# Performance work log

Hardware: AMD Instinct MI355X
Metric: run time of the kernel (lower is better)

## Reference

```python
import jax, jax.numpy as jnp
import numpy as np

THRESHOLD = 0.05
TOP_N = 512
NMS_THR = 0.6
POST_TOP_N = 100
MIN_SIZE = 0.0
N_CLASS = 8
IMG_SIZE = (256.0, 256.0, 64.0)
B, C, H, W, D = 4, 8, 128, 128, 32


def _pairwise_iou3d(b):
    # b: [K, 6] in xyzxyz; returns [K, K] volumetric IoU
    lo, hi = b[:, :3], b[:, 3:]
    ilo = jnp.maximum(lo[:, None, :], lo[None, :, :])
    ihi = jnp.minimum(hi[:, None, :], hi[None, :, :])
    inter = jnp.prod(jnp.maximum(ihi - ilo, 0.0), axis=-1)
    vol = jnp.prod(jnp.maximum(hi - lo, 0.0), axis=-1)
    return inter / (vol[:, None] + vol[None, :] - inter + 1e-9)


def _nms_keep(boxes, scores, thr):
    # greedy NMS; scores == -1 marks invalid entries. Returns bool keep mask [K].
    K = boxes.shape[0]
    order = jnp.argsort(-scores)
    b = boxes[order]
    s = scores[order]
    iou = _pairwise_iou3d(b)
    idx = jnp.arange(K)

    def body(i, keep):
        sup = (iou[i] > thr) & keep[i] & (idx > i)
        return keep & ~sup

    keep = jax.lax.fori_loop(0, K, body, s > 0.0)
    return jnp.zeros(K, dtype=bool).at[order].set(keep)


def _forward(location, cls_pred, box_pred, center_pred):
    Bb, Cc = cls_pred.shape[0], cls_pred.shape[1]
    N = cls_pred.shape[2] * cls_pred.shape[3] * cls_pred.shape[4]
    # [B, C, H, W, D] -> [B, N, C]
    cls = jax.nn.sigmoid(cls_pred).transpose(0, 2, 3, 4, 1).reshape(Bb, N, Cc)
    ctr = jax.nn.sigmoid(center_pred).transpose(0, 2, 3, 4, 1).reshape(Bb, N)
    box = box_pred.transpose(0, 2, 3, 4, 1).reshape(Bb, N, 6)

    candid = cls > THRESHOLD                      # [B, N, C]
    scores = cls * ctr[:, :, None]                # centerness-weighted
    flat = jnp.where(candid, scores, -1.0).reshape(Bb, N * Cc)
    vals, idx = jax.lax.top_k(flat, TOP_N)        # fixed-size stand-in for mask+topk
    valid = vals > 0.0                            # matches torch clamp(count, top_n)

    loc_idx = idx // Cc                           # flattened spatial location
    class_id = idx % Cc + 1                       # labels are 1-based
    bsel = jnp.take_along_axis(box, loc_idx[..., None], axis=1)   # [B, K, 6]
    lsel = location[loc_idx]                                      # [B, K, 3]
    det = jnp.concatenate([lsel - bsel[..., :3], lsel + bsel[..., 3:]], axis=-1)

    # BoxList.clip to image volume
    full = jnp.concatenate([jnp.asarray(IMG_SIZE), jnp.asarray(IMG_SIZE)]).astype(det.dtype) - 1.0
    det = jnp.clip(det, 0.0, full)

    score = jnp.where(valid, jnp.sqrt(jnp.where(valid, vals, 1.0)), 0.0)

    # remove_small_boxes
    sides = det[..., 3:] - det[..., :3]
    valid = valid & jnp.all(sides >= MIN_SIZE, axis=-1)

    # per-class greedy NMS (decisions are non-differentiable; torch detaches anyway)
    det_ng = jax.lax.stop_gradient(det)
    score_ng = jax.lax.stop_gradient(score)

    def per_image(b_i, s_i, c_i, v_i):
        def per_class(j):
            m = v_i & (c_i == j)
            return _nms_keep(b_i, jnp.where(m, s_i, -1.0), NMS_THR) & m
        return jnp.any(jax.vmap(per_class)(jnp.arange(1, N_CLASS + 1)), axis=0)

    valid = jax.vmap(per_image)(det_ng, score_ng, class_id, valid)

    # post_top_n selection (kthvalue threshold == keep top post_top_n scores)
    fv, fi = jax.lax.top_k(jnp.where(valid, score_ng, -1.0), POST_TOP_N)
    fvalid = fv > 0.0
    fbox = jnp.take_along_axis(det, fi[..., None], axis=1) * fvalid[..., None]
    fscore = jnp.where(fvalid, jnp.take_along_axis(score, fi, axis=1), 0.0)
    flabel = jnp.where(fvalid, jnp.take_along_axis(class_id, fi, axis=1), 0)
    return fbox, fscore, flabel, fvalid


def setup_inputs() -> dict:
    key = jax.random.key(0)
    k1, k2, k3, k4 = jax.random.split(key, 4)
    N = H * W * D
    location = jax.random.uniform(k1, (N, 3), dtype=jnp.float32) * jnp.asarray(IMG_SIZE, jnp.float32)
    cls_pred = jax.random.normal(k2, (B, C, H, W, D), dtype=jnp.float32) - 2.0  # realistic logits
    box_pred = jax.random.uniform(k3, (B, 6, H, W, D), dtype=jnp.float32) * 20.0  # positive extents
    center_pred = jax.random.normal(k4, (B, 1, H, W, D), dtype=jnp.float32)
    return {"location": location, "cls_pred": cls_pred, "box_pred": box_pred, "center_pred": center_pred}


def reference(location, cls_pred, box_pred, center_pred):
    return _forward(location, cls_pred, box_pred, center_pred)
```

## Files before the change

### kernel.cpp

```cpp
#include <hip/hip_runtime.h>

#define NB 4
#define NC 8
#define NLOC 524288
#define TOPN 512
#define POST 100
#define NBIN 8192
#define SELBINS 4096
#define SCAP 4096
#define CAP 16384
#define LCAP 2048
#define NMS_THR 0.6f
#define CAND_THR 0.05f
#define SPEC_THR 0.5f

typedef unsigned long long ull;

#define OFF_CNT    0
#define OFF_OVF    16
#define OFF_KEYS   64
#define ZERO_BYTES 32

__device__ __forceinline__ float sigmoidf_(float x) {
    return 1.0f / (1.0f + expf(-x));
}

__global__ __launch_bounds__(256) void gather_spec(const float* __restrict__ cls,
                                                   const float* __restrict__ ctr,
                                                   ull* __restrict__ keys,
                                                   unsigned int* __restrict__ counts,
                                                   unsigned int* __restrict__ ovf) {
    __shared__ ull lkeys[LCAP];
    __shared__ unsigned int lcnt;
    __shared__ unsigned int lbase;
    const int b = blockIdx.y;
    if (threadIdx.x == 0) lcnt = 0;
    __syncthreads();

    const int n0 = (blockIdx.x * blockDim.x + threadIdx.x) * 4;
    const float4 cv = *(const float4*)(ctr + (size_t)b * NLOC + n0);
    float4 cl[NC];
    #pragma unroll
    for (int c = 0; c < NC; ++c)
        cl[c] = *(const float4*)(cls + ((size_t)b * NC + c) * NLOC + n0);

    #pragma unroll
    for (int j = 0; j < 4; ++j) {
        bool any = false;
        #pragma unroll
        for (int c = 0; c < NC; ++c) any |= (((const float*)&cl[c])[j] > 0.0f);
        if (any) {
            const float sc = sigmoidf_(((const float*)&cv)[j]);
            #pragma unroll
            for (int c = 0; c < NC; ++c) {
                const float x = ((const float*)&cl[c])[j];
                if (x > 0.0f) {
                    const float p = sigmoidf_(x) * sc;
                    if (p > SPEC_THR) {
                        const unsigned pos = atomicAdd(&lcnt, 1u);
                        if (pos < LCAP) {
                            const unsigned flat = (unsigned)((n0 + j) * NC + c);
                            lkeys[pos] = ((ull)__float_as_uint(p) << 32) | (unsigned)(~flat);
                        }
                    }
                }
            }
        }
    }
    __syncthreads();
    const unsigned m = lcnt;
    if (threadIdx.x == 0) {
        const unsigned stored = (m > LCAP) ? LCAP : m;
        lbase = atomicAdd(&counts[b], stored);
        if (m > LCAP) ovf[b] = 1;
    }
    __syncthreads();
    const unsigned stored = (m > LCAP) ? LCAP : m;
    const unsigned base = lbase;
    for (unsigned i = threadIdx.x; i < stored; i += blockDim.x) {
        const unsigned pos = base + i;
        if (pos < CAP) keys[(size_t)b * CAP + pos] = lkeys[i];
    }
}

__global__ __launch_bounds__(1024) void select_nms_kernel(const float* __restrict__ cls,
                                                          const float* __restrict__ ctr,
                                                          ull* __restrict__ keys,
                                                          unsigned int* __restrict__ counts,
                                                          const unsigned int* __restrict__ ovf,
                                                          const float* __restrict__ loc,
                                                          const float* __restrict__ box,
                                                          float* __restrict__ out) {
    __shared__ union SU {
        struct { unsigned int hist[SELBINS]; ull surv[SCAP]; } sel;
        unsigned int fhist[NBIN];
        struct { float sd[TOPN * 6]; float ss[TOPN]; int scl[TOPN];
                 int keep[TOPN]; int clist[NC][TOPN]; int wcnt[NC]; } nms;
    } u;
    __shared__ ull tk[TOPN];
    __shared__ unsigned int scnt;
    __shared__ int cut_s;

    const int b = blockIdx.x, t = threadIdx.x;

    {
        const unsigned cnt0 = counts[b];
        const bool bad = !(cnt0 >= TOPN && cnt0 <= CAP && ovf[b] == 0);
        if (bad) {
            for (int i = t; i < NBIN; i += 1024) u.fhist[i] = 0;
            __syncthreads();
            for (int n = t; n < NLOC; n += 1024) {
                const float sc = sigmoidf_(ctr[(size_t)b * NLOC + n]);
                #pragma unroll
                for (int c = 0; c < NC; ++c) {
                    const float s = sigmoidf_(cls[((size_t)b * NC + c) * NLOC + n]);
                    if (s > CAND_THR) atomicAdd(&u.fhist[__float_as_uint(s * sc) >> 17], 1u);
                }
            }
            __syncthreads();
            if (t == 0) {
                unsigned cum = 0; int bin = 0;
                for (int i = NBIN - 1; i >= 0; --i) {
                    cum += u.fhist[i];
                    if (cum >= TOPN) { bin = i; break; }
                }
                cut_s = bin;
                counts[b] = 0;
            }
            __syncthreads();
            const unsigned cb2 = (unsigned)cut_s;
            for (int n = t; n < NLOC; n += 1024) {
                const float sc = sigmoidf_(ctr[(size_t)b * NLOC + n]);
                #pragma unroll
                for (int c = 0; c < NC; ++c) {
                    const float s = sigmoidf_(cls[((size_t)b * NC + c) * NLOC + n]);
                    if (s > CAND_THR) {
                        const unsigned bits = __float_as_uint(s * sc);
                        if ((bits >> 17) >= cb2) {
                            const unsigned pos = atomicAdd(&counts[b], 1u);
                            if (pos < CAP)
                                keys[(size_t)b * CAP + pos] =
                                    ((ull)bits << 32) | (unsigned)(~(unsigned)(n * NC + c));
                        }
                    }
                }
            }
        }
    }
    __syncthreads();

    const int M = (int)min(counts[b], (unsigned)CAP);

    for (int i = t; i < SELBINS; i += 1024) u.sel.hist[i] = 0;
    if (t == 0) scnt = 0;
    if (t < TOPN) tk[t] = 0;
    __syncthreads();
    for (int i = t; i < M; i += 1024) {
        const unsigned hi = (unsigned)(keys[(size_t)b * CAP + i] >> 32);
        const int off = (int)hi - 0x3F000000;
        int bin = (off < 0) ? 0 : (off >> 11);
        if (bin > SELBINS - 1) bin = SELBINS - 1;
        atomicAdd(&u.sel.hist[bin], 1u);
    }
    __syncthreads();

    if (t < 64) {
        unsigned s = 0;
        for (int i = 0; i < 64; ++i)
            s += u.sel.hist[t * 64 + ((i + t) & 63)];
        unsigned suf = s;
        #pragma unroll
        for (int d = 1; d < 64; d <<= 1) {
            const unsigned o = __shfl_down(suf, d);
            suf += (t + d < 64) ? o : 0u;
        }
        const ull mask = __ballot(suf >= TOPN);
        unsigned nxt = __shfl_down(suf, 1);
        if (t == 63) nxt = 0;
        if (mask == 0ull) {
            if (t == 0) cut_s = 0;
        } else {
            const int L = 63 - __builtin_clzll(mask);
            if (t == L) {
                unsigned cum = nxt;
                int c = L * 64;
                for (int i = 63; i >= 0; --i) {
                    cum += u.sel.hist[L * 64 + i];
                    if (cum >= TOPN) { c = L * 64 + i; break; }
                }
                cut_s = c;
            }
        }
    }
    __syncthreads();

    const int cb = cut_s;
    for (int i = t; i < M; i += 1024) {
        const ull k = keys[(size_t)b * CAP + i];
        const unsigned hi = (unsigned)(k >> 32);
        const int off = (int)hi - 0x3F000000;
        int bin = (off < 0) ? 0 : (off >> 11);
        if (bin > SELBINS - 1) bin = SELBINS - 1;
        if (bin >= cb) {
            const unsigned p = atomicAdd(&scnt, 1u);
            if (p < SCAP) u.sel.surv[p] = k;
        }
    }
    __syncthreads();

    const unsigned sc_final = scnt;
    if (sc_final <= (unsigned)SCAP) {
        const int S = (int)sc_final;
        for (int i = t; i < S; i += 1024) {
            const ull ke = u.sel.surv[i];
            int r = 0;
            for (int j = 0; j < S; ++j) r += (u.sel.surv[j] > ke) ? 1 : 0;
            if (r < TOPN) tk[r] = ke;
        }
    } else {
        for (int i = t; i < M; i += 1024) {
            const ull ke = keys[(size_t)b * CAP + i];
            int r = 0;
            for (int j = 0; j < M; ++j) r += (keys[(size_t)b * CAP + j] > ke) ? 1 : 0;
            if (r < TOPN) tk[r] = ke;
        }
    }
    __syncthreads();

    volatile int* keep = u.nms.keep;
    if (t < TOPN) {
        const ull k = tk[t];
        const unsigned bits = (unsigned)(k >> 32);
        const float val = __uint_as_float(bits);
        int valid = (val > 0.0f) ? 1 : 0;
        const unsigned flat = ~(unsigned)(k & 0xffffffffu);
        int n = 0, c = 0;
        if (valid) { n = (int)(flat >> 3); c = (int)(flat & 7u); }
        const float lx = loc[n * 3 + 0], ly = loc[n * 3 + 1], lz = loc[n * 3 + 2];
        const float* bp = box + (size_t)b * 6 * NLOC + n;
        const float b0 = bp[0];
        const float b1 = bp[(size_t)NLOC];
        const float b2 = bp[2 * (size_t)NLOC];
        const float b3 = bp[3 * (size_t)NLOC];
        const float b4 = bp[4 * (size_t)NLOC];
        const float b5 = bp[5 * (size_t)NLOC];
        const float d0 = fminf(fmaxf(lx - b0, 0.0f), 255.0f);
        const float d1 = fminf(fmaxf(ly - b1, 0.0f), 255.0f);
        const float d2 = fminf(fmaxf(lz - b2, 0.0f), 63.0f);
        const float d3 = fminf(fmaxf(lx + b3, 0.0f), 255.0f);
        const float d4 = fminf(fmaxf(ly + b4, 0.0f), 255.0f);
        const float d5 = fminf(fmaxf(lz + b5, 0.0f), 63.0f);
        if (d3 - d0 < 0.0f || d4 - d1 < 0.0f || d5 - d2 < 0.0f) valid = 0;
        u.nms.sd[t * 6 + 0] = d0; u.nms.sd[t * 6 + 1] = d1; u.nms.sd[t * 6 + 2] = d2;
        u.nms.sd[t * 6 + 3] = d3; u.nms.sd[t * 6 + 4] = d4; u.nms.sd[t * 6 + 5] = d5;
        u.nms.ss[t] = (val > 0.0f) ? sqrtf(val) : 0.0f;
        u.nms.scl[t] = c + 1;
        keep[t] = valid;
    }
    __syncthreads();

    if (t < TOPN) {
        const int w = t >> 6, lane = t & 63;
        const int myclass = w + 1;
        const float* sd = u.nms.sd;
        int cnt = 0;
        for (int j0 = 0; j0 < TOPN; j0 += 64) {
            const int j = j0 + lane;
            const bool pred = (u.nms.scl[j] == myclass) && (keep[j] != 0);
            const ull m = __ballot(pred);
            if (pred) {
                const int pos = cnt + __popcll(m & ((1ull << lane) - 1ull));
                u.nms.clist[w][pos] = j;
            }
            cnt += __popcll(m);
        }
        __threadfence_block();

        for (int i = 0; i < cnt; ++i) {
            const int gi = u.nms.clist[w][i];
            if (!keep[gi]) continue;
            const float lx0 = sd[gi * 6 + 0], ly0 = sd[gi * 6 + 1], lz0 = sd[gi * 6 + 2];
            const float hx0 = sd[gi * 6 + 3], hy0 = sd[gi * 6 + 4], hz0 = sd[gi * 6 + 5];
            const float vol0 = fmaxf(hx0 - lx0, 0.0f) * fmaxf(hy0 - ly0, 0.0f) * fmaxf(hz0 - lz0, 0.0f);
            for (int e = i + 1 + lane; e < cnt; e += 64) {
                const int gj = u.nms.clist[w][e];
                if (keep[gj]) {
                    const float lx1 = sd[gj * 6 + 0], ly1 = sd[gj * 6 + 1], lz1 = sd[gj * 6 + 2];
                    const float hx1 = sd[gj * 6 + 3], hy1 = sd[gj * 6 + 4], hz1 = sd[gj * 6 + 5];
                    const float ix = fminf(hx0, hx1) - fmaxf(lx0, lx1);
                    const float iy = fminf(hy0, hy1) - fmaxf(ly0, ly1);
                    const float iz = fminf(hz0, hz1) - fmaxf(lz0, lz1);
                    const float inter = fmaxf(ix, 0.0f) * fmaxf(iy, 0.0f) * fmaxf(iz, 0.0f);
                    const float vol1 = fmaxf(hx1 - lx1, 0.0f) * fmaxf(hy1 - ly1, 0.0f) * fmaxf(hz1 - lz1, 0.0f);
                    const float iou = inter / (vol0 + vol1 - inter + 1e-9f);
                    if (iou > NMS_THR) keep[gj] = 0;
                }
            }
            __threadfence_block();
        }
    }
    __syncthreads();

    if (t < TOPN) {
        const int w = t >> 6, lane = t & 63;
        const ull km = __ballot(keep[t] != 0);
        if (lane == 0) u.nms.wcnt[w] = __popcll(km);
        __threadfence_block();
        (void)km;
    }
    __syncthreads();
    if (t < TOPN) {
        const int w = t >> 6, lane = t & 63;
        const ull km = __ballot(keep[t] != 0);
        int before = 0, total = 0;
        #pragma unroll
        for (int w2 = 0; w2 < NC; ++w2) {
            total += u.nms.wcnt[w2];
            if (w2 < w) before += u.nms.wcnt[w2];
        }
        const int myrank = before + __popcll(km & ((1ull << lane) - 1ull));

        float* fbox = out;
        float* fscore = out + NB * POST * 6;
        float* flabel = out + NB * POST * 7;
        float* fvalid = out + NB * POST * 8;

        if (keep[t] && myrank < POST) {
            #pragma unroll
            for (int k = 0; k < 6; ++k) fbox[(b * POST + myrank) * 6 + k] = u.nms.sd[t * 6 + k];
            fscore[b * POST + myrank] = u.nms.ss[t];
            flabel[b * POST + myrank] = (float)u.nms.scl[t];
            fvalid[b * POST + myrank] = 1.0f;
        }
        const int tc = (total < POST) ? total : POST;
        if (t >= tc && t < POST) {
            #pragma unroll
            for (int k = 0; k < 6; ++k) fbox[(b * POST + t) * 6 + k] = 0.0f;
            fscore[b * POST + t] = 0.0f;
            flabel[b * POST + t] = 0.0f;
            fvalid[b * POST + t] = 0.0f;
        }
    }
}

extern "C" void kernel_launch(void* const* d_in, const int* in_sizes, int n_in,
                              void* d_out, int out_size, void* d_ws, size_t ws_size,
                              hipStream_t stream) {
    const float* location = (const float*)d_in[0];
    const float* cls_pred = (const float*)d_in[1];
    const float* box_pred = (const float*)d_in[2];
    const float* ctr_pred = (const float*)d_in[3];

    char* ws = (char*)d_ws;
    unsigned int* counts = (unsigned int*)(ws + OFF_CNT);
    unsigned int* ovf    = (unsigned int*)(ws + OFF_OVF);
    ull*          keys   = (ull*)(ws + OFF_KEYS);

    hipMemsetAsync(d_ws, 0, ZERO_BYTES, stream);

    gather_spec<<<dim3(NLOC / 1024, NB), 256, 0, stream>>>(cls_pred, ctr_pred, keys, counts, ovf);
    select_nms_kernel<<<NB, 1024, 0, stream>>>(cls_pred, ctr_pred, keys, counts, ovf,
                                               location, box_pred, (float*)d_out);
}
```

Before: 100.7 us.

## Register-cache keys, wave-local register NMS, 8-wide gather, fast exp

The gather kernel now has each thread process 8 locations instead of 4, halving the grid, and sigmoid uses the fast __expf intrinsic. The select kernel loads all CAP keys into registers once with 128-bit loads, so the histogram and survivor passes no longer read global memory twice. Per-class NMS keeps each box in registers and broadcasts the pivot box by shuffle with a ballot-tracked keep mask when a class has at most 128 candidates, replacing the shared-memory volatile loop. Risks: the fast exp can change scores near thresholds, and holding 16 keys per thread raises register pressure in a 1024-thread block.

```diff
diff --git a/kernel.cpp b/kernel.cpp
--- a/kernel.cpp
+++ b/kernel.cpp
@@ -9,6 +9,7 @@
 #define SELBINS 4096
 #define SCAP 4096
 #define CAP 16384
+#define KPT 16
 #define LCAP 2048
 #define NMS_THR 0.6f
 #define CAND_THR 0.05f
@@ -22,7 +23,7 @@
 #define ZERO_BYTES 32
 
 __device__ __forceinline__ float sigmoidf_(float x) {
-    return 1.0f / (1.0f + expf(-x));
+    return 1.0f / (1.0f + __expf(-x));
 }
 
 __global__ __launch_bounds__(256) void gather_spec(const float* __restrict__ cls,
@@ -37,30 +38,41 @@
     if (threadIdx.x == 0) lcnt = 0;
     __syncthreads();
 
-    const int n0 = (blockIdx.x * blockDim.x + threadIdx.x) * 4;
-    const float4 cv = *(const float4*)(ctr + (size_t)b * NLOC + n0);
-    float4 cl[NC];
+    const int n0 = (blockIdx.x * blockDim.x + threadIdx.x) * 8;
+    const float4* cvp = (const float4*)(ctr + (size_t)b * NLOC + n0);
+    const float4 cv0 = cvp[0], cv1 = cvp[1];
+    float4 cl0[NC], cl1[NC];
     #pragma unroll
-    for (int c = 0; c < NC; ++c)
-        cl[c] = *(const float4*)(cls + ((size_t)b * NC + c) * NLOC + n0);
+    for (int c = 0; c < NC; ++c) {
+        const float4* p = (const float4*)(cls + ((size_t)b * NC + c) * NLOC + n0);
+        cl0[c] = p[0];
+        cl1[c] = p[1];
+    }
 
     #pragma unroll
-    for (int j = 0; j < 4; ++j) {
-        bool any = false;
-        #pragma unroll
-        for (int c = 0; c < NC; ++c) any |= (((const float*)&cl[c])[j] > 0.0f);
-        if (any) {
-            const float sc = sigmoidf_(((const float*)&cv)[j]);
+    for (int h = 0; h < 2; ++h) {
+        const float4 cv = h ? cv1 : cv0;
+        #pragma unroll
+        for (int j = 0; j < 4; ++j) {
+            bool any = false;
             #pragma unroll
             for (int c = 0; c < NC; ++c) {
-                const float x = ((const float*)&cl[c])[j];
-                if (x > 0.0f) {
-                    const float p = sigmoidf_(x) * sc;
-                    if (p > SPEC_THR) {
-                        const unsigned pos = atomicAdd(&lcnt, 1u);
-                        if (pos < LCAP) {
-                            const unsigned flat = (unsigned)((n0 + j) * NC + c);
-                            lkeys[pos] = ((ull)__float_as_uint(p) << 32) | (unsigned)(~flat);
+                const float x = h ? ((const float*)&cl1[c])[j] : ((const float*)&cl0[c])[j];
+                any |= (x > 0.0f);
+            }
+            if (any) {
+                const float sc = sigmoidf_(((const float*)&cv)[j]);
+                #pragma unroll
+                for (int c = 0; c < NC; ++c) {
+                    const float x = h ? ((const float*)&cl1[c])[j] : ((const float*)&cl0[c])[j];
+                    if (x > 0.0f) {
+                        const float p = sigmoidf_(x) * sc;
+                        if (p > SPEC_THR) {
+                            const unsigned pos = atomicAdd(&lcnt, 1u);
+                            if (pos < LCAP) {
+                                const unsigned flat = (unsigned)((n0 + h * 4 + j) * NC + c);
+                                lkeys[pos] = ((ull)__float_as_uint(p) << 32) | (unsigned)(~flat);
+                            }
                         }
                     }
                 }
@@ -81,6 +93,16 @@
         const unsigned pos = base + i;
         if (pos < CAP) keys[(size_t)b * CAP + pos] = lkeys[i];
     }
+}
+
+__device__ __forceinline__ float iou3d_(const float* a, const float* bx) {
+    const float ix = fminf(a[3], bx[3]) - fmaxf(a[0], bx[0]);
+    const float iy = fminf(a[4], bx[4]) - fmaxf(a[1], bx[1]);
+    const float iz = fminf(a[5], bx[5]) - fmaxf(a[2], bx[2]);
+    const float inter = fmaxf(ix, 0.0f) * fmaxf(iy, 0.0f) * fmaxf(iz, 0.0f);
+    const float v0 = fmaxf(a[3] - a[0], 0.0f) * fmaxf(a[4] - a[1], 0.0f) * fmaxf(a[5] - a[2], 0.0f);
+    const float v1 = fmaxf(bx[3] - bx[0], 0.0f) * fmaxf(bx[4] - bx[1], 0.0f) * fmaxf(bx[5] - bx[2], 0.0f);
+    return inter / (v0 + v1 - inter + 1e-9f);
 }
 
 __global__ __launch_bounds__(1024) void select_nms_kernel(const float* __restrict__ cls,
@@ -145,22 +167,41 @@
                     }
                 }
             }
+            __threadfence();
         }
     }
     __syncthreads();
 
     const int M = (int)min(counts[b], (unsigned)CAP);
+
+    ull kr[KPT];
+    {
+        const ulonglong2* kb = (const ulonglong2*)(keys + (size_t)b * CAP);
+        #pragma unroll
+        for (int p = 0; p < KPT / 2; ++p) {
+            const ulonglong2 v = kb[p * 1024 + t];
+            kr[2 * p] = v.x;
+            kr[2 * p + 1] = v.y;
+        }
+    }
 
     for (int i = t; i < SELBINS; i += 1024) u.sel.hist[i] = 0;
     if (t == 0) scnt = 0;
     if (t < TOPN) tk[t] = 0;
     __syncthreads();
-    for (int i = t; i < M; i += 1024) {
-        const unsigned hi = (unsigned)(keys[(size_t)b * CAP + i] >> 32);
-        const int off = (int)hi - 0x3F000000;
-        int bin = (off < 0) ? 0 : (off >> 11);
-        if (bin > SELBINS - 1) bin = SELBINS - 1;
-        atomicAdd(&u.sel.hist[bin], 1u);
+    #pragma unroll
+    for (int p = 0; p < KPT / 2; ++p) {
+        #pragma unroll
+        for (int q = 0; q < 2; ++q) {
+            const int i = 2 * (p * 1024 + t) + q;
+            if (i < M) {
+                const unsigned hi = (unsigned)(kr[2 * p + q] >> 32);
+                const int off = (int)hi - 0x3F000000;
+                int bin = (off < 0) ? 0 : (off >> 11);
+                if (bin > SELBINS - 1) bin = SELBINS - 1;
+                atomicAdd(&u.sel.hist[bin], 1u);
+            }
+        }
     }
     __syncthreads();
 
@@ -195,15 +236,22 @@
     __syncthreads();
 
     const int cb = cut_s;
-    for (int i = t; i < M; i += 1024) {
-        const ull k = keys[(size_t)b * CAP + i];
-        const unsigned hi = (unsigned)(k >> 32);
-        const int off = (int)hi - 0x3F000000;
-        int bin = (off < 0) ? 0 : (off >> 11);
-        if (bin > SELBINS - 1) bin = SELBINS - 1;
-        if (bin >= cb) {
-            const unsigned p = atomicAdd(&scnt, 1u);
-            if (p < SCAP) u.sel.surv[p] = k;
+    #pragma unroll
+    for (int p = 0; p < KPT / 2; ++p) {
+        #pragma unroll
+        for (int q = 0; q < 2; ++q) {
+            const int i = 2 * (p * 1024 + t) + q;
+            if (i < M) {
+                const ull k = kr[2 * p + q];
+                const unsigned hi = (unsigned)(k >> 32);
+                const int off = (int)hi - 0x3F000000;
+                int bin = (off < 0) ? 0 : (off >> 11);
+                if (bin > SELBINS - 1) bin = SELBINS - 1;
+                if (bin >= cb) {
+                    const unsigned p2 = atomicAdd(&scnt, 1u);
+                    if (p2 < SCAP) u.sel.surv[p2] = k;
+                }
+            }
         }
     }
     __syncthreads();
@@ -227,7 +275,6 @@
     }
     __syncthreads();
 
-    volatile int* keep = u.nms.keep;
     if (t < TOPN) {
         const ull k = tk[t];
         const unsigned bits = (unsigned)(k >> 32);
@@ -255,18 +302,17 @@
         u.nms.sd[t * 6 + 3] = d3; u.nms.sd[t * 6 + 4] = d4; u.nms.sd[t * 6 + 5] = d5;
         u.nms.ss[t] = (val > 0.0f) ? sqrtf(val) : 0.0f;
         u.nms.scl[t] = c + 1;
-        keep[t] = valid;
+        u.nms.keep[t] = valid;
     }
     __syncthreads();
 
     if (t < TOPN) {
         const int w = t >> 6, lane = t & 63;
         const int myclass = w + 1;
-        const float* sd = u.nms.sd;
         int cnt = 0;
         for (int j0 = 0; j0 < TOPN; j0 += 64) {
             const int j = j0 + lane;
-            const bool pred = (u.nms.scl[j] == myclass) && (keep[j] != 0);
+            const bool pred = (u.nms.scl[j] == myclass) && (u.nms.keep[j] != 0);
             const ull m = __ballot(pred);
             if (pred) {
                 const int pos = cnt + __popcll(m & ((1ull << lane) - 1ull));
@@ -276,42 +322,63 @@
         }
         __threadfence_block();
 
-        for (int i = 0; i < cnt; ++i) {
-            const int gi = u.nms.clist[w][i];
-            if (!keep[gi]) continue;
-            const float lx0 = sd[gi * 6 + 0], ly0 = sd[gi * 6 + 1], lz0 = sd[gi * 6 + 2];
-            const float hx0 = sd[gi * 6 + 3], hy0 = sd[gi * 6 + 4], hz0 = sd[gi * 6 + 5];
-            const float vol0 = fmaxf(hx0 - lx0, 0.0f) * fmaxf(hy0 - ly0, 0.0f) * fmaxf(hz0 - lz0, 0.0f);
-            for (int e = i + 1 + lane; e < cnt; e += 64) {
-                const int gj = u.nms.clist[w][e];
-                if (keep[gj]) {
-                    const float lx1 = sd[gj * 6 + 0], ly1 = sd[gj * 6 + 1], lz1 = sd[gj * 6 + 2];
-                    const float hx1 = sd[gj * 6 + 3], hy1 = sd[gj * 6 + 4], hz1 = sd[gj * 6 + 5];
-                    const float ix = fminf(hx0, hx1) - fmaxf(lx0, lx1);
-                    const float iy = fminf(hy0, hy1) - fmaxf(ly0, ly1);
-                    const float iz = fminf(hz0, hz1) - fmaxf(lz0, lz1);
-                    const float inter = fmaxf(ix, 0.0f) * fmaxf(iy, 0.0f) * fmaxf(iz, 0.0f);
-                    const float vol1 = fmaxf(hx1 - lx1, 0.0f) * fmaxf(hy1 - ly1, 0.0f) * fmaxf(hz1 - lz1, 0.0f);
-                    const float iou = inter / (vol0 + vol1 - inter + 1e-9f);
-                    if (iou > NMS_THR) keep[gj] = 0;
-                }
-            }
-            __threadfence_block();
+        if (cnt <= 128) {
+            const int g0 = (lane < cnt) ? u.nms.clist[w][lane] : -1;
+            const int g1 = (lane + 64 < cnt) ? u.nms.clist[w][lane + 64] : -1;
+            float B0[6], B1[6];
+            #pragma unroll
+            for (int q = 0; q < 6; ++q) {
+                B0[q] = (g0 >= 0) ? u.nms.sd[g0 * 6 + q] : 0.0f;
+                B1[q] = (g1 >= 0) ? u.nms.sd[g1 * 6 + q] : 0.0f;
+            }
+            bool a0 = (g0 >= 0), a1 = (g1 >= 0);
+            ull m0 = __ballot(a0), m1 = __ballot(a1);
+            for (int i = 0; i < cnt; ++i) {
+                const int ki = i >> 6, li = i & 63;
+                const ull mi = ki ? m1 : m0;
+                if (!((mi >> li) & 1ull)) continue;
+                float pb[6];
+                #pragma unroll
+                for (int q = 0; q < 6; ++q) pb[q] = __shfl(ki ? B1[q] : B0[q], li);
+                if (a0 && lane > i)      { if (iou3d_(B0, pb) > NMS_THR) a0 = false; }
+                if (a1 && lane + 64 > i) { if (iou3d_(B1, pb) > NMS_THR) a1 = false; }
+                m0 = __ballot(a0); m1 = __ballot(a1);
+            }
+            if (g0 >= 0 && !a0) u.nms.keep[g0] = 0;
+            if (g1 >= 0 && !a1) u.nms.keep[g1] = 0;
+        } else {
+            volatile int* vkeep = u.nms.keep;
+            const float* sd = u.nms.sd;
+            for (int i = 0; i < cnt; ++i) {
+                const int gi = u.nms.clist[w][i];
+                if (!vkeep[gi]) continue;
+                float pb[6];
+                #pragma unroll
+                for (int q = 0; q < 6; ++q) pb[q] = sd[gi * 6 + q];
+                for (int e = i + 1 + lane; e < cnt; e += 64) {
+                    const int gj = u.nms.clist[w][e];
+                    if (vkeep[gj]) {
+                        float cb_[6];
+                        #pragma unroll
+                        for (int q = 0; q < 6; ++q) cb_[q] = sd[gj * 6 + q];
+                        if (iou3d_(cb_, pb) > NMS_THR) vkeep[gj] = 0;
+                    }
+                }
+                __threadfence_block();
+            }
         }
     }
     __syncthreads();
 
     if (t < TOPN) {
         const int w = t >> 6, lane = t & 63;
-        const ull km = __ballot(keep[t] != 0);
+        const ull km = __ballot(u.nms.keep[t] != 0);
         if (lane == 0) u.nms.wcnt[w] = __popcll(km);
-        __threadfence_block();
-        (void)km;
     }
     __syncthreads();
     if (t < TOPN) {
         const int w = t >> 6, lane = t & 63;
-        const ull km = __ballot(keep[t] != 0);
+        const ull km = __ballot(u.nms.keep[t] != 0);
         int before = 0, total = 0;
         #pragma unroll
         for (int w2 = 0; w2 < NC; ++w2) {
@@ -325,7 +392,7 @@
         float* flabel = out + NB * POST * 7;
         float* fvalid = out + NB * POST * 8;
 
-        if (keep[t] && myrank < POST) {
+        if (u.nms.keep[t] && myrank < POST) {
             #pragma unroll
             for (int k = 0; k < 6; ++k) fbox[(b * POST + myrank) * 6 + k] = u.nms.sd[t * 6 + k];
             fscore[b * POST + myrank] = u.nms.ss[t];
@@ -358,7 +425,7 @@
 
     hipMemsetAsync(d_ws, 0, ZERO_BYTES, stream);
 
-    gather_spec<<<dim3(NLOC / 1024, NB), 256, 0, stream>>>(cls_pred, ctr_pred, keys, counts, ovf);
+    gather_spec<<<dim3(NLOC / 2048, NB), 256, 0, stream>>>(cls_pred, ctr_pred, keys, counts, ovf);
     select_nms_kernel<<<NB, 1024, 0, stream>>>(cls_pred, ctr_pred, keys, counts, ovf,
                                                location, box_pred, (float*)d_out);
 }
```

Result: faster. 85.96 us (-14.7%).
